# Optimization experiments

Measured on AMD Instinct MI355X. Metric: run time of the kernel, lower is better.

Reference implementation:

```python
import jax, jax.numpy as jnp
import numpy as np

B, D, N, L = 64, 8, 2048, 64
MISS_RATE = 0.2


def setup_inputs() -> dict:
    key = jax.random.key(0)
    k1, k2 = jax.random.split(key)
    x = jax.random.normal(k1, (B, D, N, L), dtype=jnp.float32)
    miss = jax.random.uniform(k2, (B, D, N, L)) < MISS_RATE
    # missing entries are encoded as -inf, exactly as the torch module expects
    x = jnp.where(miss, -jnp.inf, x)
    return {"x": x}


def reference(x) -> jnp.ndarray:
    # Faithful vectorization of Imputer(type='MEAN').forward.
    # Torch semantics: iterate missing indices in lexicographic (b,d,n,s) order,
    # cache the mean by key (batch, node). Hence for each (b,n) the mean used is
    # the observed-seq mean of row x[b, d0, n, :], where d0 is the SMALLEST dim
    # index that has at least one missing entry at that (b,n). NaN/empty -> 0.
    mask = x == -jnp.inf                           # [B,D,N,L] missing positions
    row_missing = mask.any(axis=-1)                # [B,D,N]
    d0 = jnp.argmax(row_missing, axis=1)           # [B,N], first dim with missing
    x_d0 = jnp.take_along_axis(x, d0[:, None, :, None], axis=1)[:, 0]  # [B,N,L]
    obs = x_d0 != -jnp.inf                         # observed entries of that row
    cnt = obs.sum(axis=-1)                         # [B,N]
    s = jnp.where(obs, x_d0, 0.0).sum(axis=-1)     # [B,N]
    mean = jnp.where(cnt > 0, s / jnp.maximum(cnt, 1), 0.0)  # [B,N]
    return jnp.where(mask, mean[:, None, :, None], x)
```

## Files before the change

kernel.cpp:

```cpp
#include <hip/hip_runtime.h>
#include <stdint.h>

#define B_ 64
#define D_ 8
#define N_ 2048
#define L_ 64

__device__ __forceinline__ bool is_ninf(float v) {
    return __float_as_uint(v) == 0xFF800000u;
}

__global__ __launch_bounds__(256) void imputer_kernel(const float* __restrict__ x,
                                                      float* __restrict__ out) {
    const int lane = threadIdx.x & 63;
    const int wave = threadIdx.x >> 6;
    const int p    = blockIdx.x * 4 + wave;
    const int b    = p >> 11;
    const int n    = p & (N_ - 1);

    const size_t rstride = (size_t)N_ * L_;
    const size_t base    = (size_t)b * (D_ * rstride) + (size_t)n * L_;

    const int g = lane >> 4;
    const int c = lane & 15;

    const float* p0 = x + base + (size_t)g       * rstride + (size_t)c * 4;
    const float* p1 = x + base + (size_t)(g + 4) * rstride + (size_t)c * 4;

    float4 v0 = *(const float4*)p0;
    float4 v1 = *(const float4*)p1;

    const bool m0x = is_ninf(v0.x), m0y = is_ninf(v0.y), m0z = is_ninf(v0.z), m0w = is_ninf(v0.w);
    const bool m1x = is_ninf(v1.x), m1y = is_ninf(v1.y), m1z = is_ninf(v1.z), m1w = is_ninf(v1.w);

    const unsigned long long bal0 = __ballot(m0x | m0y | m0z | m0w);
    const unsigned long long bal1 = __ballot(m1x | m1y | m1z | m1w);

    unsigned mask8 = 0;
#pragma unroll
    for (int d = 0; d < 4; ++d) {
        if ((bal0 >> (16 * d)) & 0xFFFFull) mask8 |= 1u << d;
        if ((bal1 >> (16 * d)) & 0xFFFFull) mask8 |= 1u << (d + 4);
    }

    float mean = 0.0f;
    if (mask8) {
        const int d0 = __ffs(mask8) - 1;
        const int h0 = d0 >> 2;
        const int g0 = d0 & 3;

        const float4 vv = h0 ? v1 : v0;
        float ps = 0.0f, pc = 0.0f;
        if (g == g0) {
            if (!is_ninf(vv.x)) { ps += vv.x; pc += 1.0f; }
            if (!is_ninf(vv.y)) { ps += vv.y; pc += 1.0f; }
            if (!is_ninf(vv.z)) { ps += vv.z; pc += 1.0f; }
            if (!is_ninf(vv.w)) { ps += vv.w; pc += 1.0f; }
        }
#pragma unroll
        for (int off = 32; off; off >>= 1) {
            ps += __shfl_xor(ps, off, 64);
            pc += __shfl_xor(pc, off, 64);
        }
        mean = (pc > 0.0f) ? (ps / pc) : 0.0f;
    }

    v0.x = m0x ? mean : v0.x;
    v0.y = m0y ? mean : v0.y;
    v0.z = m0z ? mean : v0.z;
    v0.w = m0w ? mean : v0.w;
    v1.x = m1x ? mean : v1.x;
    v1.y = m1y ? mean : v1.y;
    v1.z = m1z ? mean : v1.z;
    v1.w = m1w ? mean : v1.w;

    float* q0 = out + base + (size_t)g       * rstride + (size_t)c * 4;
    float* q1 = out + base + (size_t)(g + 4) * rstride + (size_t)c * 4;
    *(float4*)q0 = v0;
    *(float4*)q1 = v1;
}

extern "C" void kernel_launch(void* const* d_in, const int* in_sizes, int n_in,
                              void* d_out, int out_size, void* d_ws, size_t ws_size,
                              hipStream_t stream) {
    const float* x = (const float*)d_in[0];
    float* out = (float*)d_out;
    const int pairs = B_ * N_;
    const int blocks = pairs / 4;
    imputer_kernel<<<blocks, 256, 0, stream>>>(x, out);
}
```

Measured before the change: 419.4 us.

## Process 16 (b,n) pairs per wave with nontemporal stores and ballot counts

Each wave now loops over 16 consecutive (b,n) pairs instead of handling one, with the loop unrolled by 4 so several loads are in flight. Outputs are written with nontemporal stores to avoid polluting cache. The observed count comes from per-component ballots and popcount, and the sum needs only a 16-lane reduction plus readlane, which shortens the shuffle chain. The risks are fewer blocks, which lowers parallelism, and higher register pressure from the unrolling.

```diff
diff --git a/kernel.cpp b/kernel.cpp
--- a/kernel.cpp
+++ b/kernel.cpp
@@ -5,6 +5,11 @@
 #define D_ 8
 #define N_ 2048
 #define L_ 64
+
+#define WAVES_PER_BLOCK 4
+#define PAIRS_PER_WAVE 16
+
+typedef float f32x4 __attribute__((ext_vector_type(4)));
 
 __device__ __forceinline__ bool is_ninf(float v) {
     return __float_as_uint(v) == 0xFF800000u;
@@ -14,70 +19,84 @@
                                                       float* __restrict__ out) {
     const int lane = threadIdx.x & 63;
     const int wave = threadIdx.x >> 6;
-    const int p    = blockIdx.x * 4 + wave;
-    const int b    = p >> 11;
-    const int n    = p & (N_ - 1);
+    const int wgid = blockIdx.x * WAVES_PER_BLOCK + wave;
+    const int p0i  = wgid * PAIRS_PER_WAVE;
+    const int b    = p0i >> 11;
+    const int n0   = p0i & (N_ - 1);
 
     const size_t rstride = (size_t)N_ * L_;
-    const size_t base    = (size_t)b * (D_ * rstride) + (size_t)n * L_;
+    const size_t base    = (size_t)b * (D_ * rstride) + (size_t)n0 * L_;
 
     const int g = lane >> 4;
     const int c = lane & 15;
 
-    const float* p0 = x + base + (size_t)g       * rstride + (size_t)c * 4;
-    const float* p1 = x + base + (size_t)(g + 4) * rstride + (size_t)c * 4;
+    const float* pa = x   + base + (size_t)g       * rstride + (size_t)c * 4;
+    const float* pb = x   + base + (size_t)(g + 4) * rstride + (size_t)c * 4;
+    float*       qa = out + base + (size_t)g       * rstride + (size_t)c * 4;
+    float*       qb = out + base + (size_t)(g + 4) * rstride + (size_t)c * 4;
 
-    float4 v0 = *(const float4*)p0;
-    float4 v1 = *(const float4*)p1;
+#pragma unroll 4
+    for (int it = 0; it < PAIRS_PER_WAVE; ++it) {
+        f32x4 v0 = *(const f32x4*)(pa + (size_t)it * L_);
+        f32x4 v1 = *(const f32x4*)(pb + (size_t)it * L_);
 
-    const bool m0x = is_ninf(v0.x), m0y = is_ninf(v0.y), m0z = is_ninf(v0.z), m0w = is_ninf(v0.w);
-    const bool m1x = is_ninf(v1.x), m1y = is_ninf(v1.y), m1z = is_ninf(v1.z), m1w = is_ninf(v1.w);
+        const bool m0x = is_ninf(v0[0]), m0y = is_ninf(v0[1]), m0z = is_ninf(v0[2]), m0w = is_ninf(v0[3]);
+        const bool m1x = is_ninf(v1[0]), m1y = is_ninf(v1[1]), m1z = is_ninf(v1[2]), m1w = is_ninf(v1[3]);
 
-    const unsigned long long bal0 = __ballot(m0x | m0y | m0z | m0w);
-    const unsigned long long bal1 = __ballot(m1x | m1y | m1z | m1w);
+        const unsigned long long bx0 = __ballot(m0x), by0 = __ballot(m0y), bz0 = __ballot(m0z), bw0 = __ballot(m0w);
+        const unsigned long long bx1 = __ballot(m1x), by1 = __ballot(m1y), bz1 = __ballot(m1z), bw1 = __ballot(m1w);
+        const unsigned long long any0 = bx0 | by0 | bz0 | bw0;
+        const unsigned long long any1 = bx1 | by1 | bz1 | bw1;
 
-    unsigned mask8 = 0;
+        unsigned mask8 = 0;
 #pragma unroll
-    for (int d = 0; d < 4; ++d) {
-        if ((bal0 >> (16 * d)) & 0xFFFFull) mask8 |= 1u << d;
-        if ((bal1 >> (16 * d)) & 0xFFFFull) mask8 |= 1u << (d + 4);
+        for (int d = 0; d < 4; ++d) {
+            if ((any0 >> (16 * d)) & 0xFFFFull) mask8 |= 1u << d;
+            if ((any1 >> (16 * d)) & 0xFFFFull) mask8 |= 1u << (d + 4);
+        }
+
+        float mean = 0.0f;
+        if (mask8) {
+            const int d0 = __ffs(mask8) - 1;
+            const int h0 = d0 >> 2;
+            const int g0 = d0 & 3;
+            const int sh = 16 * g0;
+
+            const unsigned fx = (unsigned)((h0 ? bx1 : bx0) >> sh) & 0xFFFFu;
+            const unsigned fy = (unsigned)((h0 ? by1 : by0) >> sh) & 0xFFFFu;
+            const unsigned fz = (unsigned)((h0 ? bz1 : bz0) >> sh) & 0xFFFFu;
+            const unsigned fw = (unsigned)((h0 ? bw1 : bw0) >> sh) & 0xFFFFu;
+            const int cnt = 64 - (__popc(fx) + __popc(fy) + __popc(fz) + __popc(fw));
+
+            float psl = 0.0f;
+            if (g == g0) {
+                const f32x4 vv = h0 ? v1 : v0;
+                if (!is_ninf(vv[0])) psl += vv[0];
+                if (!is_ninf(vv[1])) psl += vv[1];
+                if (!is_ninf(vv[2])) psl += vv[2];
+                if (!is_ninf(vv[3])) psl += vv[3];
+            }
+            psl += __shfl_xor(psl, 1, 64);
+            psl += __shfl_xor(psl, 2, 64);
+            psl += __shfl_xor(psl, 4, 64);
+            psl += __shfl_xor(psl, 8, 64);
+            const float ps = __uint_as_float(
+                __builtin_amdgcn_readlane(__float_as_uint(psl), sh));
+            mean = (cnt > 0) ? ps / (float)cnt : 0.0f;
+        }
+
+        v0[0] = m0x ? mean : v0[0];
+        v0[1] = m0y ? mean : v0[1];
+        v0[2] = m0z ? mean : v0[2];
+        v0[3] = m0w ? mean : v0[3];
+        v1[0] = m1x ? mean : v1[0];
+        v1[1] = m1y ? mean : v1[1];
+        v1[2] = m1z ? mean : v1[2];
+        v1[3] = m1w ? mean : v1[3];
+
+        __builtin_nontemporal_store(v0, (f32x4*)(qa + (size_t)it * L_));
+        __builtin_nontemporal_store(v1, (f32x4*)(qb + (size_t)it * L_));
     }
-
-    float mean = 0.0f;
-    if (mask8) {
-        const int d0 = __ffs(mask8) - 1;
-        const int h0 = d0 >> 2;
-        const int g0 = d0 & 3;
-
-        const float4 vv = h0 ? v1 : v0;
-        float ps = 0.0f, pc = 0.0f;
-        if (g == g0) {
-            if (!is_ninf(vv.x)) { ps += vv.x; pc += 1.0f; }
-            if (!is_ninf(vv.y)) { ps += vv.y; pc += 1.0f; }
-            if (!is_ninf(vv.z)) { ps += vv.z; pc += 1.0f; }
-            if (!is_ninf(vv.w)) { ps += vv.w; pc += 1.0f; }
-        }
-#pragma unroll
-        for (int off = 32; off; off >>= 1) {
-            ps += __shfl_xor(ps, off, 64);
-            pc += __shfl_xor(pc, off, 64);
-        }
-        mean = (pc > 0.0f) ? (ps / pc) : 0.0f;
-    }
-
-    v0.x = m0x ? mean : v0.x;
-    v0.y = m0y ? mean : v0.y;
-    v0.z = m0z ? mean : v0.z;
-    v0.w = m0w ? mean : v0.w;
-    v1.x = m1x ? mean : v1.x;
-    v1.y = m1y ? mean : v1.y;
-    v1.z = m1z ? mean : v1.z;
-    v1.w = m1w ? mean : v1.w;
-
-    float* q0 = out + base + (size_t)g       * rstride + (size_t)c * 4;
-    float* q1 = out + base + (size_t)(g + 4) * rstride + (size_t)c * 4;
-    *(float4*)q0 = v0;
-    *(float4*)q1 = v1;
 }
 
 extern "C" void kernel_launch(void* const* d_in, const int* in_sizes, int n_in,
@@ -85,7 +104,6 @@
                               hipStream_t stream) {
     const float* x = (const float*)d_in[0];
     float* out = (float*)d_out;
-    const int pairs = B_ * N_;
-    const int blocks = pairs / 4;
+    const int blocks = (B_ * N_) / (WAVES_PER_BLOCK * PAIRS_PER_WAVE);
     imputer_kernel<<<blocks, 256, 0, stream>>>(x, out);
 }
```

Result: slower. 476.4 us (+13.6%).
